# Performance work log

Hardware: AMD Instinct MI355X
Metric: run time of the kernel (lower is better)

Reference implementation:

```python
import jax, jax.numpy as jnp
import numpy as np

N_NODES = 100000
N_EDGES = 3200000
IN_F, HID, N_CLS = 10, 64, 10
NEG_SLOPE = 0.01  # torch default for F.leaky_relu


def gcn_conv(h, src, dst, W, b, n_nodes):
    h = h @ W  # transform first (small feature dim -> cheap)
    # self loops
    loop = jnp.arange(n_nodes, dtype=src.dtype)
    s = jnp.concatenate([src, loop])
    d = jnp.concatenate([dst, loop])
    deg = jax.ops.segment_sum(jnp.ones_like(d, dtype=h.dtype), d, num_segments=n_nodes)
    dinv = jnp.where(deg > 0, jax.lax.rsqrt(deg), 0.0)
    norm = dinv[s] * dinv[d]  # [E+N]
    msg = h[s] * norm[:, None]  # gather + scale
    out = jax.ops.segment_sum(msg, d, num_segments=n_nodes)  # scatter-add
    return out + b


def setup_inputs() -> dict:
    key = jax.random.key(0)
    ks = jax.random.split(key, 10)
    x = jax.random.normal(ks[0], (N_NODES, IN_F), dtype=jnp.float32)
    edge_index = jax.random.randint(ks[1], (2, N_EDGES), 0, N_NODES, dtype=jnp.int64)
    def glorot(k, fan_in, fan_out):
        lim = np.sqrt(6.0 / (fan_in + fan_out))
        return jax.random.uniform(k, (fan_in, fan_out), jnp.float32, -lim, lim)
    W1 = glorot(ks[2], IN_F, HID)
    b1 = jnp.zeros((HID,), jnp.float32)
    W2 = glorot(ks[3], HID, HID)
    b2 = jnp.zeros((HID,), jnp.float32)
    W3 = glorot(ks[4], HID, HID)
    b3 = jnp.zeros((HID,), jnp.float32)
    Wfc = glorot(ks[5], HID, N_CLS)
    bfc = jnp.zeros((N_CLS,), jnp.float32)
    return {"x": x, "edge_index": edge_index, "W1": W1, "b1": b1,
            "W2": W2, "b2": b2, "W3": W3, "b3": b3, "Wfc": Wfc, "bfc": bfc}


def reference(x, edge_index, W1, b1, W2, b2, W3, b3, Wfc, bfc):
    src, dst = edge_index[0], edge_index[1]
    n = x.shape[0]
    h = jax.nn.leaky_relu(gcn_conv(x, src, dst, W1, b1, n), NEG_SLOPE)
    h = jax.nn.leaky_relu(gcn_conv(h, src, dst, W2, b2, n), NEG_SLOPE)
    h = jax.nn.leaky_relu(gcn_conv(h, src, dst, W3, b3, n), NEG_SLOPE)
    return h @ Wfc + bfc
```

## Files before the change

### kernel.cpp

```cpp
#include <hip/hip_runtime.h>
#include <hip/hip_fp16.h>

#define N_NODES_C 100000
#define N_EDGES_C 3200000
#define IN_F_C 10
#define HID_C 64
#define N_CLS_C 10
#define NEG_SLOPE_C 0.01f

#define NBUCK 98
#define BCAP  36864
#define TILE  2048

typedef _Float16 f16x2 __attribute__((ext_vector_type(2)));

__device__ __forceinline__ float fdot2(unsigned int a, unsigned int b, float c) {
#if defined(__has_builtin) && __has_builtin(__builtin_amdgcn_fdot2)
    return __builtin_amdgcn_fdot2(__builtin_bit_cast(f16x2, a), __builtin_bit_cast(f16x2, b), c, false);
#else
    __half2 ah = __builtin_bit_cast(__half2, a), bh = __builtin_bit_cast(__half2, b);
    float2 af = __half22float2(ah), bf = __half22float2(bh);
    return c + af.x * bf.x + af.y * bf.y;
#endif
}

__global__ __launch_bounds__(256) void k_bucket(const int* __restrict__ src,
                                                const int* __restrict__ dst,
                                                int* __restrict__ bcur,
                                                int* __restrict__ pairs, int E) {
    __shared__ int lcnt[NBUCK];
    __shared__ int gbase[NBUCK];
    const int t = threadIdx.x;
    for (int i = t; i < NBUCK; i += 256) lcnt[i] = 0;
    __syncthreads();
    const int base = blockIdx.x * TILE;
    int p[8], r[8], nb[8];
#pragma unroll
    for (int i = 0; i < 8; ++i) {
        int e = base + t + i * 256;
        if (e < E) {
            int s = src[e], d = dst[e];
            int b = d >> 10;
            nb[i] = b;
            p[i] = (s << 10) | (d & 1023);
            r[i] = atomicAdd(&lcnt[b], 1);
        }
    }
    __syncthreads();
    for (int i = t; i < NBUCK; i += 256)
        gbase[i] = lcnt[i] ? atomicAdd(&bcur[i], lcnt[i]) : 0;
    __syncthreads();
#pragma unroll
    for (int i = 0; i < 8; ++i) {
        int e = base + t + i * 256;
        if (e < E) {
            int pos = gbase[nb[i]] + r[i];
            if (pos < BCAP) pairs[nb[i] * BCAP + pos] = p[i];
        }
    }
}

__global__ __launch_bounds__(1024) void k_build(const int* __restrict__ pairs,
                                                const int* __restrict__ bcur,
                                                int* __restrict__ row_ptr,
                                                float* __restrict__ dinv,
                                                int* __restrict__ col) {
    __shared__ int hist[1024];
    __shared__ int sm[1024];
    __shared__ int bs[128];
    const int b = blockIdx.x;
    const int t = threadIdx.x;
    const int n = min(bcur[b], BCAP);
    const int* pp = pairs + b * BCAP;

    if (t < 128) bs[t] = (t < NBUCK) ? bcur[t] : 0;
    __syncthreads();
    for (int off = 1; off < 128; off <<= 1) {
        int u = 0;
        if (t < 128 && t >= off) u = bs[t - off];
        __syncthreads();
        if (t < 128) bs[t] += u;
        __syncthreads();
    }
    const int base = (b > 0) ? bs[b - 1] : 0;

    hist[t] = 0;
    __syncthreads();
    for (int i = t; i < n; i += 1024) atomicAdd(&hist[pp[i] & 1023], 1);
    __syncthreads();
    int c = hist[t];
    sm[t] = c;
    __syncthreads();
    for (int off = 1; off < 1024; off <<= 1) {
        int u = (t >= off) ? sm[t - off] : 0;
        __syncthreads();
        sm[t] += u;
        __syncthreads();
    }
    int rp = base + sm[t] - c;
    int gnode = (b << 10) + t;
    if (gnode < N_NODES_C) {
        row_ptr[gnode] = rp;
        dinv[gnode] = rsqrtf((float)(c + 1));
        if (gnode == N_NODES_C - 1) row_ptr[N_NODES_C] = rp + c;
    }
    __syncthreads();
    sm[t] = rp;
    __syncthreads();
    for (int i = t; i < n; i += 1024) {
        int p = pp[i];
        int idx = atomicAdd(&sm[p & 1023], 1);
        col[idx] = p >> 10;
    }
}

__global__ __launch_bounds__(256) void k_mm0(const float* __restrict__ x,
                                             const float* __restrict__ W,
                                             const float* __restrict__ dinv,
                                             __half* __restrict__ hs, int n) {
    __shared__ float4 W4[IN_F_C * 16];
    const int t = threadIdx.x;
    for (int i = t; i < IN_F_C * 16; i += 256) {
        int k = i >> 4, f4 = i & 15;
        W4[i] = ((const float4*)(W + k * HID_C))[f4];
    }
    __syncthreads();
    int idx = blockIdx.x * 256 + t;
    if (idx >= n * 16) return;
    int nn = idx >> 4, f4 = idx & 15;
    const float* row = x + nn * IN_F_C;
    float4 acc = make_float4(0.f, 0.f, 0.f, 0.f);
#pragma unroll
    for (int k = 0; k < IN_F_C; ++k) {
        float xv = row[k];
        float4 w = W4[k * 16 + f4];
        acc.x += xv * w.x; acc.y += xv * w.y; acc.z += xv * w.z; acc.w += xv * w.w;
    }
    float di = dinv[nn];
    ((__half2*)hs)[(nn << 5) + 2 * f4]     = __floats2half2_rn(acc.x * di, acc.y * di);
    ((__half2*)hs)[(nn << 5) + 2 * f4 + 1] = __floats2half2_rn(acc.z * di, acc.w * di);
}

__global__ __launch_bounds__(256) void k_wcvt(const float* __restrict__ W, uint4* __restrict__ wh) {
    int i = blockIdx.x * 256 + threadIdx.x;
    if (i >= 8 * HID_C) return;
    int k8 = i >> 6, f = i & 63;
    __half2 h[4];
#pragma unroll
    for (int j = 0; j < 4; ++j)
        h[j] = __floats2half2_rn(W[(8 * k8 + 2 * j) * HID_C + f],
                                 W[(8 * k8 + 2 * j + 1) * HID_C + f]);
    wh[i] = *(uint4*)h;
}

__global__ __launch_bounds__(256) void k_wcvtf(const float* __restrict__ W, float4* __restrict__ wq) {
    int i = threadIdx.x;
    if (i >= 16 * N_CLS_C) return;
    int k4 = i / N_CLS_C, f = i - k4 * N_CLS_C;
    wq[i] = make_float4(W[(4 * k4 + 0) * N_CLS_C + f], W[(4 * k4 + 1) * N_CLS_C + f],
                        W[(4 * k4 + 2) * N_CLS_C + f], W[(4 * k4 + 3) * N_CLS_C + f]);
}

__global__ __launch_bounds__(512) void k_gft(const int* __restrict__ row_ptr,
                                             const int* __restrict__ col,
                                             const __half* __restrict__ hsrc,
                                             const float* __restrict__ dinv,
                                             const float* __restrict__ bias,
                                             const uint4* __restrict__ wh,
                                             __half* __restrict__ hnext, int n) {
    __shared__ uint4 WhL[8 * HID_C];
    __shared__ __half2 rowh[8][32];
    const int t = threadIdx.x;
    WhL[t] = wh[t];
    __syncthreads();

    const int lane = t & 63;
    const int wid  = t >> 6;
    const int g    = lane >> 4;
    const int fl   = lane & 15;
    const int d = (blockIdx.x << 3) + wid;
    if (d >= n) return;
    const int beg = row_ptr[d];
    const int end = row_ptr[d + 1];
    const float2* hsv = (const float2*)hsrc;

    float4 acc = make_float4(0.f, 0.f, 0.f, 0.f);
    if (g == 0) {
        float2 raw = hsv[(d << 4) + fl];
        float2 a0 = __half22float2(*(__half2*)&raw.x);
        float2 a1 = __half22float2(*(__half2*)&raw.y);
        acc = make_float4(a0.x, a0.y, a1.x, a1.y);
    }
    int e = beg;
    for (; e + 15 < end; e += 16) {
        int s0 = col[e + g];
        int s1 = col[e + 4 + g];
        int s2 = col[e + 8 + g];
        int s3 = col[e + 12 + g];
        float2 r0 = hsv[(s0 << 4) + fl];
        float2 r1 = hsv[(s1 << 4) + fl];
        float2 r2 = hsv[(s2 << 4) + fl];
        float2 r3 = hsv[(s3 << 4) + fl];
        float2 a0 = __half22float2(*(__half2*)&r0.x), a1 = __half22float2(*(__half2*)&r0.y);
        float2 b0 = __half22float2(*(__half2*)&r1.x), b1 = __half22float2(*(__half2*)&r1.y);
        float2 c0 = __half22float2(*(__half2*)&r2.x), c1 = __half22float2(*(__half2*)&r2.y);
        float2 d0 = __half22float2(*(__half2*)&r3.x), d1 = __half22float2(*(__half2*)&r3.y);
        acc.x += (a0.x + b0.x) + (c0.x + d0.x);
        acc.y += (a0.y + b0.y) + (c0.y + d0.y);
        acc.z += (a1.x + b1.x) + (c1.x + d1.x);
        acc.w += (a1.y + b1.y) + (c1.y + d1.y);
    }
    for (; e < end; e += 4) {
        int i = e + g;
        if (i < end) {
            float2 r = hsv[(col[i] << 4) + fl];
            float2 a0 = __half22float2(*(__half2*)&r.x);
            float2 a1 = __half22float2(*(__half2*)&r.y);
            acc.x += a0.x; acc.y += a0.y; acc.z += a1.x; acc.w += a1.y;
        }
    }
    acc.x += __shfl_xor(acc.x, 16, 64); acc.y += __shfl_xor(acc.y, 16, 64);
    acc.z += __shfl_xor(acc.z, 16, 64); acc.w += __shfl_xor(acc.w, 16, 64);
    acc.x += __shfl_xor(acc.x, 32, 64); acc.y += __shfl_xor(acc.y, 32, 64);
    acc.z += __shfl_xor(acc.z, 32, 64); acc.w += __shfl_xor(acc.w, 32, 64);

    const float di = dinv[d];
    if (g == 0) {
        float4 bb = ((const float4*)bias)[fl];
        float4 v;
        v.x = acc.x * di + bb.x; v.y = acc.y * di + bb.y;
        v.z = acc.z * di + bb.z; v.w = acc.w * di + bb.w;
        v.x = v.x > 0.f ? v.x : NEG_SLOPE_C * v.x;
        v.y = v.y > 0.f ? v.y : NEG_SLOPE_C * v.y;
        v.z = v.z > 0.f ? v.z : NEG_SLOPE_C * v.z;
        v.w = v.w > 0.f ? v.w : NEG_SLOPE_C * v.w;
        rowh[wid][2 * fl]     = __floats2half2_rn(v.x, v.y);
        rowh[wid][2 * fl + 1] = __floats2half2_rn(v.z, v.w);
    }
    {
        float s = 0.f;
        const uint4* rq = (const uint4*)rowh[wid];
#pragma unroll
        for (int k8 = 0; k8 < 8; ++k8) {
            uint4 wv = WhL[(k8 << 6) + lane];
            uint4 rv = rq[k8];
            s = fdot2(rv.x, wv.x, s);
            s = fdot2(rv.y, wv.y, s);
            s = fdot2(rv.z, wv.z, s);
            s = fdot2(rv.w, wv.w, s);
        }
        hnext[(d << 6) + lane] = __float2half(s * di);
    }
}

__global__ __launch_bounds__(512) void k_gfc(const int* __restrict__ row_ptr,
                                             const int* __restrict__ col,
                                             const __half* __restrict__ hsrc,
                                             const float* __restrict__ dinv,
                                             const float* __restrict__ bias,
                                             const float4* __restrict__ wq,
                                             const float* __restrict__ bn,
                                             float* __restrict__ out, int n) {
    __shared__ float4 Ws4[16 * N_CLS_C];
    __shared__ float rowbuf[8][64];
    const int t = threadIdx.x;
    if (t < 16 * N_CLS_C) Ws4[t] = wq[t];
    __syncthreads();

    const int lane = t & 63;
    const int wid  = t >> 6;
    const int g    = lane >> 4;
    const int fl   = lane & 15;
    const int d = (blockIdx.x << 3) + wid;
    if (d >= n) return;
    const int beg = row_ptr[d];
    const int end = row_ptr[d + 1];
    const float2* hsv = (const float2*)hsrc;

    float4 acc = make_float4(0.f, 0.f, 0.f, 0.f);
    if (g == 0) {
        float2 raw = hsv[(d << 4) + fl];
        float2 a0 = __half22float2(*(__half2*)&raw.x);
        float2 a1 = __half22float2(*(__half2*)&raw.y);
        acc = make_float4(a0.x, a0.y, a1.x, a1.y);
    }
    int e = beg;
    for (; e + 15 < end; e += 16) {
        int s0 = col[e + g];
        int s1 = col[e + 4 + g];
        int s2 = col[e + 8 + g];
        int s3 = col[e + 12 + g];
        float2 r0 = hsv[(s0 << 4) + fl];
        float2 r1 = hsv[(s1 << 4) + fl];
        float2 r2 = hsv[(s2 << 4) + fl];
        float2 r3 = hsv[(s3 << 4) + fl];
        float2 a0 = __half22float2(*(__half2*)&r0.x), a1 = __half22float2(*(__half2*)&r0.y);
        float2 b0 = __half22float2(*(__half2*)&r1.x), b1 = __half22float2(*(__half2*)&r1.y);
        float2 c0 = __half22float2(*(__half2*)&r2.x), c1 = __half22float2(*(__half2*)&r2.y);
        float2 d0 = __half22float2(*(__half2*)&r3.x), d1 = __half22float2(*(__half2*)&r3.y);
        acc.x += (a0.x + b0.x) + (c0.x + d0.x);
        acc.y += (a0.y + b0.y) + (c0.y + d0.y);
        acc.z += (a1.x + b1.x) + (c1.x + d1.x);
        acc.w += (a1.y + b1.y) + (c1.y + d1.y);
    }
    for (; e < end; e += 4) {
        int i = e + g;
        if (i < end) {
            float2 r = hsv[(col[i] << 4) + fl];
            float2 a0 = __half22float2(*(__half2*)&r.x);
            float2 a1 = __half22float2(*(__half2*)&r.y);
            acc.x += a0.x; acc.y += a0.y; acc.z += a1.x; acc.w += a1.y;
        }
    }
    acc.x += __shfl_xor(acc.x, 16, 64); acc.y += __shfl_xor(acc.y, 16, 64);
    acc.z += __shfl_xor(acc.z, 16, 64); acc.w += __shfl_xor(acc.w, 16, 64);
    acc.x += __shfl_xor(acc.x, 32, 64); acc.y += __shfl_xor(acc.y, 32, 64);
    acc.z += __shfl_xor(acc.z, 32, 64); acc.w += __shfl_xor(acc.w, 32, 64);

    const float di = dinv[d];
    if (g == 0) {
        float4 bb = ((const float4*)bias)[fl];
        float4 v;
        v.x = acc.x * di + bb.x; v.y = acc.y * di + bb.y;
        v.z = acc.z * di + bb.z; v.w = acc.w * di + bb.w;
        v.x = v.x > 0.f ? v.x : NEG_SLOPE_C * v.x;
        v.y = v.y > 0.f ? v.y : NEG_SLOPE_C * v.y;
        v.z = v.z > 0.f ? v.z : NEG_SLOPE_C * v.z;
        v.w = v.w > 0.f ? v.w : NEG_SLOPE_C * v.w;
        ((float4*)rowbuf[wid])[fl] = v;
    }
    if (lane < N_CLS_C) {
        float s = bn[lane];
        const float4* rb = (const float4*)rowbuf[wid];
#pragma unroll
        for (int k4 = 0; k4 < 16; ++k4) {
            float4 r4 = rb[k4];
            float4 w4 = Ws4[k4 * N_CLS_C + lane];
            s += r4.x * w4.x + r4.y * w4.y + r4.z * w4.z + r4.w * w4.w;
        }
        out[d * N_CLS_C + lane] = s;
    }
}

extern "C" void kernel_launch(void* const* d_in, const int* in_sizes, int n_in,
                              void* d_out, int out_size, void* d_ws, size_t ws_size,
                              hipStream_t stream) {
    const float* x   = (const float*)d_in[0];
    const int*   ei  = (const int*)d_in[1];
    const float* W1  = (const float*)d_in[2];
    const float* b1  = (const float*)d_in[3];
    const float* W2  = (const float*)d_in[4];
    const float* b2  = (const float*)d_in[5];
    const float* W3  = (const float*)d_in[6];
    const float* b3  = (const float*)d_in[7];
    const float* Wfc = (const float*)d_in[8];
    const float* bfc = (const float*)d_in[9];
    float* out = (float*)d_out;

    const int N = N_NODES_C;
    const int E = N_EDGES_C;
    const int* src = ei;
    const int* dst = ei + E;

    float*  dinv    = (float*)d_ws;
    int*    bcur    = (int*)(dinv + N);
    int*    row_ptr = bcur + 128;
    uint4*  wh2     = (uint4*)(row_ptr + N + 4);
    uint4*  wh3     = wh2 + 512;
    float4* wfcq    = (float4*)(wh3 + 512);
    int*    col     = (int*)(wfcq + 160);
    int*    pairs   = col + E;
    __half* hsA     = (__half*)pairs;
    __half* hsB     = (__half*)(pairs + (size_t)NBUCK * BCAP);

    int gN8 = (N + 7) / 8;
    int gM0 = (N * 16 + 255) / 256;
    int gBK = (E + TILE - 1) / TILE;

    hipMemsetAsync(bcur, 0, 128 * sizeof(int), stream);
    k_bucket<<<gBK, 256, 0, stream>>>(src, dst, bcur, pairs, E);
    k_build<<<NBUCK, 1024, 0, stream>>>(pairs, bcur, row_ptr, dinv, col);

    k_wcvt<<<2, 256, 0, stream>>>(W2, wh2);
    k_wcvt<<<2, 256, 0, stream>>>(W3, wh3);
    k_wcvtf<<<1, 256, 0, stream>>>(Wfc, wfcq);

    k_mm0<<<gM0, 256, 0, stream>>>(x, W1, dinv, hsA, N);

    k_gft<<<gN8, 512, 0, stream>>>(row_ptr, col, hsA, dinv, b1, wh2, hsB, N);
    k_gft<<<gN8, 512, 0, stream>>>(row_ptr, col, hsB, dinv, b2, wh3, hsA, N);
    k_gfc<<<gN8, 512, 0, stream>>>(row_ptr, col, hsA, dinv, b3, wfcq, bfc, out, N);
}
```

Measured before the change: 395.0 us.

## Widen gather loads to 16B, per-wave bucket counters, merge prep kernels

The aggregation kernels now have each lane gather a 16-byte uint4 (8 halves) per neighbor, with 8 edges in flight per wave instead of 4. Column indices are read with nontemporal loads. The bucketing kernel splits its shared-memory counters per wavefront to cut LDS atomic contention. The memset and three weight-conversion launches are folded into one prep kernel to cut launch overhead. Wider loads mean fewer memory instructions per edge, but the shuffle reduction grows by one extra level.

```diff
diff --git a/kernel.cpp b/kernel.cpp
--- a/kernel.cpp
+++ b/kernel.cpp
@@ -24,14 +24,43 @@
 #endif
 }
 
+__global__ __launch_bounds__(256) void k_prep(const float* __restrict__ W2, const float* __restrict__ W3,
+                                              const float* __restrict__ Wfc,
+                                              uint4* __restrict__ wh2, uint4* __restrict__ wh3,
+                                              float4* __restrict__ wfq, int* __restrict__ bcur) {
+    const int b = blockIdx.x, t = threadIdx.x;
+    if (b < 2) {
+        const float* W = b ? W3 : W2;
+        uint4* wh = b ? wh3 : wh2;
+        for (int i = t; i < 8 * HID_C; i += 256) {
+            int k8 = i >> 6, f = i & 63;
+            __half2 h[4];
+#pragma unroll
+            for (int j = 0; j < 4; ++j)
+                h[j] = __floats2half2_rn(W[(8 * k8 + 2 * j) * HID_C + f],
+                                         W[(8 * k8 + 2 * j + 1) * HID_C + f]);
+            wh[i] = *(uint4*)h;
+        }
+    } else if (b == 2) {
+        if (t < 16 * N_CLS_C) {
+            int k4 = t / N_CLS_C, f = t - k4 * N_CLS_C;
+            wfq[t] = make_float4(Wfc[(4 * k4 + 0) * N_CLS_C + f], Wfc[(4 * k4 + 1) * N_CLS_C + f],
+                                 Wfc[(4 * k4 + 2) * N_CLS_C + f], Wfc[(4 * k4 + 3) * N_CLS_C + f]);
+        }
+    } else {
+        if (t < 128) bcur[t] = 0;
+    }
+}
+
 __global__ __launch_bounds__(256) void k_bucket(const int* __restrict__ src,
                                                 const int* __restrict__ dst,
                                                 int* __restrict__ bcur,
                                                 int* __restrict__ pairs, int E) {
-    __shared__ int lcnt[NBUCK];
-    __shared__ int gbase[NBUCK];
-    const int t = threadIdx.x;
-    for (int i = t; i < NBUCK; i += 256) lcnt[i] = 0;
+    __shared__ int lcnt[4][NBUCK];
+    __shared__ int wb[4][NBUCK];
+    const int t = threadIdx.x;
+    const int w = t >> 6;
+    for (int i = t; i < 4 * NBUCK; i += 256) ((int*)lcnt)[i] = 0;
     __syncthreads();
     const int base = blockIdx.x * TILE;
     int p[8], r[8], nb[8];
@@ -43,18 +72,22 @@
             int b = d >> 10;
             nb[i] = b;
             p[i] = (s << 10) | (d & 1023);
-            r[i] = atomicAdd(&lcnt[b], 1);
-        }
-    }
-    __syncthreads();
-    for (int i = t; i < NBUCK; i += 256)
-        gbase[i] = lcnt[i] ? atomicAdd(&bcur[i], lcnt[i]) : 0;
+            r[i] = atomicAdd(&lcnt[w][b], 1);
+        }
+    }
+    __syncthreads();
+    for (int i = t; i < NBUCK; i += 256) {
+        int c0 = lcnt[0][i], c1 = lcnt[1][i], c2 = lcnt[2][i], c3 = lcnt[3][i];
+        int tot = c0 + c1 + c2 + c3;
+        int gb = tot ? atomicAdd(&bcur[i], tot) : 0;
+        wb[0][i] = gb; wb[1][i] = gb + c0; wb[2][i] = gb + c0 + c1; wb[3][i] = gb + c0 + c1 + c2;
+    }
     __syncthreads();
 #pragma unroll
     for (int i = 0; i < 8; ++i) {
         int e = base + t + i * 256;
         if (e < E) {
-            int pos = gbase[nb[i]] + r[i];
+            int pos = wb[w][nb[i]] + r[i];
             if (pos < BCAP) pairs[nb[i] * BCAP + pos] = p[i];
         }
     }
@@ -141,25 +174,65 @@
     ((__half2*)hs)[(nn << 5) + 2 * f4 + 1] = __floats2half2_rn(acc.z * di, acc.w * di);
 }
 
-__global__ __launch_bounds__(256) void k_wcvt(const float* __restrict__ W, uint4* __restrict__ wh) {
-    int i = blockIdx.x * 256 + threadIdx.x;
-    if (i >= 8 * HID_C) return;
-    int k8 = i >> 6, f = i & 63;
-    __half2 h[4];
-#pragma unroll
-    for (int j = 0; j < 4; ++j)
-        h[j] = __floats2half2_rn(W[(8 * k8 + 2 * j) * HID_C + f],
-                                 W[(8 * k8 + 2 * j + 1) * HID_C + f]);
-    wh[i] = *(uint4*)h;
-}
-
-__global__ __launch_bounds__(256) void k_wcvtf(const float* __restrict__ W, float4* __restrict__ wq) {
-    int i = threadIdx.x;
-    if (i >= 16 * N_CLS_C) return;
-    int k4 = i / N_CLS_C, f = i - k4 * N_CLS_C;
-    wq[i] = make_float4(W[(4 * k4 + 0) * N_CLS_C + f], W[(4 * k4 + 1) * N_CLS_C + f],
-                        W[(4 * k4 + 2) * N_CLS_C + f], W[(4 * k4 + 3) * N_CLS_C + f]);
-}
+#define ACC8(q)                                                                        \
+    {                                                                                  \
+        const __half2* hp_ = (const __half2*)&(q);                                     \
+        float2 a0_ = __half22float2(hp_[0]), a1_ = __half22float2(hp_[1]);             \
+        float2 a2_ = __half22float2(hp_[2]), a3_ = __half22float2(hp_[3]);             \
+        accA.x += a0_.x; accA.y += a0_.y; accA.z += a1_.x; accA.w += a1_.y;            \
+        accB.x += a2_.x; accB.y += a2_.y; accB.z += a3_.x; accB.w += a3_.y;            \
+    }
+
+#define GCORE()                                                                        \
+    float4 accA = make_float4(0.f, 0.f, 0.f, 0.f), accB = accA;                        \
+    if (g8 == 0 && d < n) { uint4 q_ = hsq[(d << 3) + f8]; ACC8(q_) }                  \
+    int e = 0, end = -1;                                                               \
+    if (d < n) { e = row_ptr[d]; end = row_ptr[d + 1]; }                               \
+    for (; e + 15 < end; e += 16) {                                                    \
+        int s0_ = __builtin_nontemporal_load(col + e + g8);                            \
+        int s1_ = __builtin_nontemporal_load(col + e + 8 + g8);                        \
+        uint4 q0_ = hsq[(s0_ << 3) + f8];                                              \
+        uint4 q1_ = hsq[(s1_ << 3) + f8];                                              \
+        ACC8(q0_)                                                                      \
+        ACC8(q1_)                                                                      \
+    }                                                                                  \
+    for (; e < end; e += 8) {                                                          \
+        int i_ = e + g8;                                                               \
+        if (i_ < end) {                                                                \
+            int s_ = __builtin_nontemporal_load(col + i_);                             \
+            uint4 q_ = hsq[(s_ << 3) + f8];                                            \
+            ACC8(q_)                                                                   \
+        }                                                                              \
+    }                                                                                  \
+    accA.x += __shfl_xor(accA.x, 8, 64);  accA.y += __shfl_xor(accA.y, 8, 64);         \
+    accA.z += __shfl_xor(accA.z, 8, 64);  accA.w += __shfl_xor(accA.w, 8, 64);         \
+    accB.x += __shfl_xor(accB.x, 8, 64);  accB.y += __shfl_xor(accB.y, 8, 64);         \
+    accB.z += __shfl_xor(accB.z, 8, 64);  accB.w += __shfl_xor(accB.w, 8, 64);         \
+    accA.x += __shfl_xor(accA.x, 16, 64); accA.y += __shfl_xor(accA.y, 16, 64);        \
+    accA.z += __shfl_xor(accA.z, 16, 64); accA.w += __shfl_xor(accA.w, 16, 64);        \
+    accB.x += __shfl_xor(accB.x, 16, 64); accB.y += __shfl_xor(accB.y, 16, 64);        \
+    accB.z += __shfl_xor(accB.z, 16, 64); accB.w += __shfl_xor(accB.w, 16, 64);        \
+    accA.x += __shfl_xor(accA.x, 32, 64); accA.y += __shfl_xor(accA.y, 32, 64);        \
+    accA.z += __shfl_xor(accA.z, 32, 64); accA.w += __shfl_xor(accA.w, 32, 64);        \
+    accB.x += __shfl_xor(accB.x, 32, 64); accB.y += __shfl_xor(accB.y, 32, 64);        \
+    accB.z += __shfl_xor(accB.z, 32, 64); accB.w += __shfl_xor(accB.w, 32, 64);
+
+#define EPI_MATH()                                                                     \
+    const float4 bb0 = ((const float4*)bias)[2 * f8];                                  \
+    const float4 bb1 = ((const float4*)bias)[2 * f8 + 1];                              \
+    float4 v0, v1;                                                                     \
+    v0.x = accA.x * di + bb0.x; v0.y = accA.y * di + bb0.y;                            \
+    v0.z = accA.z * di + bb0.z; v0.w = accA.w * di + bb0.w;                            \
+    v1.x = accB.x * di + bb1.x; v1.y = accB.y * di + bb1.y;                            \
+    v1.z = accB.z * di + bb1.z; v1.w = accB.w * di + bb1.w;                            \
+    v0.x = v0.x > 0.f ? v0.x : NEG_SLOPE_C * v0.x;                                     \
+    v0.y = v0.y > 0.f ? v0.y : NEG_SLOPE_C * v0.y;                                     \
+    v0.z = v0.z > 0.f ? v0.z : NEG_SLOPE_C * v0.z;                                     \
+    v0.w = v0.w > 0.f ? v0.w : NEG_SLOPE_C * v0.w;                                     \
+    v1.x = v1.x > 0.f ? v1.x : NEG_SLOPE_C * v1.x;                                     \
+    v1.y = v1.y > 0.f ? v1.y : NEG_SLOPE_C * v1.y;                                     \
+    v1.z = v1.z > 0.f ? v1.z : NEG_SLOPE_C * v1.z;                                     \
+    v1.w = v1.w > 0.f ? v1.w : NEG_SLOPE_C * v1.w;
 
 __global__ __launch_bounds__(512) void k_gft(const int* __restrict__ row_ptr,
                                              const int* __restrict__ col,
@@ -169,88 +242,40 @@
                                              const uint4* __restrict__ wh,
                                              __half* __restrict__ hnext, int n) {
     __shared__ uint4 WhL[8 * HID_C];
-    __shared__ __half2 rowh[8][32];
+    __shared__ uint4 rowq[8][8];
     const int t = threadIdx.x;
     WhL[t] = wh[t];
     __syncthreads();
 
-    const int lane = t & 63;
-    const int wid  = t >> 6;
-    const int g    = lane >> 4;
-    const int fl   = lane & 15;
+    const int lane = t & 63, wid = t >> 6;
+    const int g8 = lane >> 3, f8 = lane & 7;
     const int d = (blockIdx.x << 3) + wid;
+    const uint4* hsq = (const uint4*)hsrc;
+
+    GCORE()
     if (d >= n) return;
-    const int beg = row_ptr[d];
-    const int end = row_ptr[d + 1];
-    const float2* hsv = (const float2*)hsrc;
-
-    float4 acc = make_float4(0.f, 0.f, 0.f, 0.f);
-    if (g == 0) {
-        float2 raw = hsv[(d << 4) + fl];
-        float2 a0 = __half22float2(*(__half2*)&raw.x);
-        float2 a1 = __half22float2(*(__half2*)&raw.y);
-        acc = make_float4(a0.x, a0.y, a1.x, a1.y);
-    }
-    int e = beg;
-    for (; e + 15 < end; e += 16) {
-        int s0 = col[e + g];
-        int s1 = col[e + 4 + g];
-        int s2 = col[e + 8 + g];
-        int s3 = col[e + 12 + g];
-        float2 r0 = hsv[(s0 << 4) + fl];
-        float2 r1 = hsv[(s1 << 4) + fl];
-        float2 r2 = hsv[(s2 << 4) + fl];
-        float2 r3 = hsv[(s3 << 4) + fl];
-        float2 a0 = __half22float2(*(__half2*)&r0.x), a1 = __half22float2(*(__half2*)&r0.y);
-        float2 b0 = __half22float2(*(__half2*)&r1.x), b1 = __half22float2(*(__half2*)&r1.y);
-        float2 c0 = __half22float2(*(__half2*)&r2.x), c1 = __half22float2(*(__half2*)&r2.y);
-        float2 d0 = __half22float2(*(__half2*)&r3.x), d1 = __half22float2(*(__half2*)&r3.y);
-        acc.x += (a0.x + b0.x) + (c0.x + d0.x);
-        acc.y += (a0.y + b0.y) + (c0.y + d0.y);
-        acc.z += (a1.x + b1.x) + (c1.x + d1.x);
-        acc.w += (a1.y + b1.y) + (c1.y + d1.y);
-    }
-    for (; e < end; e += 4) {
-        int i = e + g;
-        if (i < end) {
-            float2 r = hsv[(col[i] << 4) + fl];
-            float2 a0 = __half22float2(*(__half2*)&r.x);
-            float2 a1 = __half22float2(*(__half2*)&r.y);
-            acc.x += a0.x; acc.y += a0.y; acc.z += a1.x; acc.w += a1.y;
-        }
-    }
-    acc.x += __shfl_xor(acc.x, 16, 64); acc.y += __shfl_xor(acc.y, 16, 64);
-    acc.z += __shfl_xor(acc.z, 16, 64); acc.w += __shfl_xor(acc.w, 16, 64);
-    acc.x += __shfl_xor(acc.x, 32, 64); acc.y += __shfl_xor(acc.y, 32, 64);
-    acc.z += __shfl_xor(acc.z, 32, 64); acc.w += __shfl_xor(acc.w, 32, 64);
-
     const float di = dinv[d];
-    if (g == 0) {
-        float4 bb = ((const float4*)bias)[fl];
-        float4 v;
-        v.x = acc.x * di + bb.x; v.y = acc.y * di + bb.y;
-        v.z = acc.z * di + bb.z; v.w = acc.w * di + bb.w;
-        v.x = v.x > 0.f ? v.x : NEG_SLOPE_C * v.x;
-        v.y = v.y > 0.f ? v.y : NEG_SLOPE_C * v.y;
-        v.z = v.z > 0.f ? v.z : NEG_SLOPE_C * v.z;
-        v.w = v.w > 0.f ? v.w : NEG_SLOPE_C * v.w;
-        rowh[wid][2 * fl]     = __floats2half2_rn(v.x, v.y);
-        rowh[wid][2 * fl + 1] = __floats2half2_rn(v.z, v.w);
-    }
-    {
-        float s = 0.f;
-        const uint4* rq = (const uint4*)rowh[wid];
-#pragma unroll
-        for (int k8 = 0; k8 < 8; ++k8) {
-            uint4 wv = WhL[(k8 << 6) + lane];
-            uint4 rv = rq[k8];
-            s = fdot2(rv.x, wv.x, s);
-            s = fdot2(rv.y, wv.y, s);
-            s = fdot2(rv.z, wv.z, s);
-            s = fdot2(rv.w, wv.w, s);
-        }
-        hnext[(d << 6) + lane] = __float2half(s * di);
-    }
+    if (g8 == 0) {
+        EPI_MATH()
+        __half2 h[4];
+        h[0] = __floats2half2_rn(v0.x, v0.y);
+        h[1] = __floats2half2_rn(v0.z, v0.w);
+        h[2] = __floats2half2_rn(v1.x, v1.y);
+        h[3] = __floats2half2_rn(v1.z, v1.w);
+        rowq[wid][f8] = *(uint4*)h;
+    }
+    float s = 0.f;
+    const uint4* rq = rowq[wid];
+#pragma unroll
+    for (int k8 = 0; k8 < 8; ++k8) {
+        uint4 wv = WhL[(k8 << 6) + lane];
+        uint4 rv = rq[k8];
+        s = fdot2(rv.x, wv.x, s);
+        s = fdot2(rv.y, wv.y, s);
+        s = fdot2(rv.z, wv.z, s);
+        s = fdot2(rv.w, wv.w, s);
+    }
+    hnext[(d << 6) + lane] = __float2half(s * di);
 }
 
 __global__ __launch_bounds__(512) void k_gfc(const int* __restrict__ row_ptr,
@@ -267,67 +292,18 @@
     if (t < 16 * N_CLS_C) Ws4[t] = wq[t];
     __syncthreads();
 
-    const int lane = t & 63;
-    const int wid  = t >> 6;
-    const int g    = lane >> 4;
-    const int fl   = lane & 15;
+    const int lane = t & 63, wid = t >> 6;
+    const int g8 = lane >> 3, f8 = lane & 7;
     const int d = (blockIdx.x << 3) + wid;
+    const uint4* hsq = (const uint4*)hsrc;
+
+    GCORE()
     if (d >= n) return;
-    const int beg = row_ptr[d];
-    const int end = row_ptr[d + 1];
-    const float2* hsv = (const float2*)hsrc;
-
-    float4 acc = make_float4(0.f, 0.f, 0.f, 0.f);
-    if (g == 0) {
-        float2 raw = hsv[(d << 4) + fl];
-        float2 a0 = __half22float2(*(__half2*)&raw.x);
-        float2 a1 = __half22float2(*(__half2*)&raw.y);
-        acc = make_float4(a0.x, a0.y, a1.x, a1.y);
-    }
-    int e = beg;
-    for (; e + 15 < end; e += 16) {
-        int s0 = col[e + g];
-        int s1 = col[e + 4 + g];
-        int s2 = col[e + 8 + g];
-        int s3 = col[e + 12 + g];
-        float2 r0 = hsv[(s0 << 4) + fl];
-        float2 r1 = hsv[(s1 << 4) + fl];
-        float2 r2 = hsv[(s2 << 4) + fl];
-        float2 r3 = hsv[(s3 << 4) + fl];
-        float2 a0 = __half22float2(*(__half2*)&r0.x), a1 = __half22float2(*(__half2*)&r0.y);
-        float2 b0 = __half22float2(*(__half2*)&r1.x), b1 = __half22float2(*(__half2*)&r1.y);
-        float2 c0 = __half22float2(*(__half2*)&r2.x), c1 = __half22float2(*(__half2*)&r2.y);
-        float2 d0 = __half22float2(*(__half2*)&r3.x), d1 = __half22float2(*(__half2*)&r3.y);
-        acc.x += (a0.x + b0.x) + (c0.x + d0.x);
-        acc.y += (a0.y + b0.y) + (c0.y + d0.y);
-        acc.z += (a1.x + b1.x) + (c1.x + d1.x);
-        acc.w += (a1.y + b1.y) + (c1.y + d1.y);
-    }
-    for (; e < end; e += 4) {
-        int i = e + g;
-        if (i < end) {
-            float2 r = hsv[(col[i] << 4) + fl];
-            float2 a0 = __half22float2(*(__half2*)&r.x);
-            float2 a1 = __half22float2(*(__half2*)&r.y);
-            acc.x += a0.x; acc.y += a0.y; acc.z += a1.x; acc.w += a1.y;
-        }
-    }
-    acc.x += __shfl_xor(acc.x, 16, 64); acc.y += __shfl_xor(acc.y, 16, 64);
-    acc.z += __shfl_xor(acc.z, 16, 64); acc.w += __shfl_xor(acc.w, 16, 64);
-    acc.x += __shfl_xor(acc.x, 32, 64); acc.y += __shfl_xor(acc.y, 32, 64);
-    acc.z += __shfl_xor(acc.z, 32, 64); acc.w += __shfl_xor(acc.w, 32, 64);
-
     const float di = dinv[d];
-    if (g == 0) {
-        float4 bb = ((const float4*)bias)[fl];
-        float4 v;
-        v.x = acc.x * di + bb.x; v.y = acc.y * di + bb.y;
-        v.z = acc.z * di + bb.z; v.w = acc.w * di + bb.w;
-        v.x = v.x > 0.f ? v.x : NEG_SLOPE_C * v.x;
-        v.y = v.y > 0.f ? v.y : NEG_SLOPE_C * v.y;
-        v.z = v.z > 0.f ? v.z : NEG_SLOPE_C * v.z;
-        v.w = v.w > 0.f ? v.w : NEG_SLOPE_C * v.w;
-        ((float4*)rowbuf[wid])[fl] = v;
+    if (g8 == 0) {
+        EPI_MATH()
+        ((float4*)rowbuf[wid])[2 * f8]     = v0;
+        ((float4*)rowbuf[wid])[2 * f8 + 1] = v1;
     }
     if (lane < N_CLS_C) {
         float s = bn[lane];
@@ -377,13 +353,10 @@
     int gM0 = (N * 16 + 255) / 256;
     int gBK = (E + TILE - 1) / TILE;
 
-    hipMemsetAsync(bcur, 0, 128 * sizeof(int), stream);
+    k_prep<<<4, 256, 0, stream>>>(W2, W3, Wfc, wh2, wh3, wfcq, bcur);
+
     k_bucket<<<gBK, 256, 0, stream>>>(src, dst, bcur, pairs, E);
     k_build<<<NBUCK, 1024, 0, stream>>>(pairs, bcur, row_ptr, dinv, col);
-
-    k_wcvt<<<2, 256, 0, stream>>>(W2, wh2);
-    k_wcvt<<<2, 256, 0, stream>>>(W3, wh3);
-    k_wcvtf<<<1, 256, 0, stream>>>(Wfc, wfcq);
 
     k_mm0<<<gM0, 256, 0, stream>>>(x, W1, dinv, hsA, N);
 
```

Result: no change. 401.3 us (+1.6%).
